# Performance work log

Measured on AMD Instinct MI355X. Metric: run time of the kernel, lower is better.

Reference implementation:

```python
import jax, jax.numpy as jnp
import numpy as np
import math

B, S, D_MODEL, NHEAD, DFF = 4, 1024, 1024, 16, 4096
D_K = D_MODEL // NHEAD
EPS = 1e-5
FACTOR = 5  # ProbAttention factor


def setup_inputs() -> dict:
    key = jax.random.key(0)
    ks = jax.random.split(key, 16)
    def w(k, shape):
        return 0.02 * jax.random.normal(k, shape, jnp.float32)
    inp = {
        "tgt": jax.random.normal(ks[0], (B, S, D_MODEL), jnp.float32),
        "memory": jax.random.normal(ks[1], (B, S, D_MODEL), jnp.float32),
    }
    i = 2
    for n in ["sa_wq", "sa_wk", "sa_wv", "sa_wo", "ca_wq", "ca_wk", "ca_wv", "ca_wo"]:
        inp[n] = w(ks[i], (D_MODEL, D_MODEL)); i += 1
        inp[n.replace("_w", "_b")] = jnp.zeros((D_MODEL,), jnp.float32)
    inp["w1"] = w(ks[i], (D_MODEL, DFF)); i += 1
    inp["b1"] = jnp.zeros((DFF,), jnp.float32)
    inp["w2"] = w(ks[i], (DFF, D_MODEL)); i += 1
    inp["b2"] = jnp.zeros((D_MODEL,), jnp.float32)
    for j in (1, 2, 3):
        inp[f"bn{j}_g"] = jnp.ones((D_MODEL,), jnp.float32)
        inp[f"bn{j}_b"] = jnp.zeros((D_MODEL,), jnp.float32)
    return inp


def prob_attention(q, k, v, rng):
    # Informer ProbSparse attention, mask_flag=False. q,k,v: [B,H,L,D]
    Bq, H, Lq, D = q.shape
    Lk = k.shape[2]
    sample_k = min(FACTOR * int(math.ceil(math.log(Lk))), Lk)
    n_top = min(FACTOR * int(math.ceil(math.log(Lq))), Lq)
    # sampled key indices per query position (shared across B,H, as in Informer)
    idx = jax.random.randint(rng, (Lq, sample_k), 0, Lk)
    k_samp = k[:, :, idx, :]                                 # [B,H,Lq,sample_k,D]
    qk_samp = jnp.einsum("bhld,bhlsd->bhls", q, k_samp)
    M = qk_samp.max(-1) - qk_samp.sum(-1) / Lk               # sparsity measure [B,H,Lq]
    top_idx = jax.lax.top_k(M, n_top)[1]                     # [B,H,n_top]
    q_red = jnp.take_along_axis(q, top_idx[..., None], axis=2)  # [B,H,n_top,D]
    scores = jnp.einsum("bhud,bhkd->bhuk", q_red, k) * (1.0 / math.sqrt(D))
    attn = jax.nn.softmax(scores, axis=-1)                   # [B,H,n_top,Lk]
    # initial context: mean of V for all queries, then overwrite the top queries
    ctx = jnp.broadcast_to(v.mean(axis=2, keepdims=True), (Bq, H, Lq, D))
    upd = jnp.einsum("bhuk,bhkd->bhud", attn, v)
    b_ix = jnp.arange(Bq)[:, None, None]
    h_ix = jnp.arange(H)[None, :, None]
    return ctx.at[b_ix, h_ix, top_idx].set(upd)


def mha(xq, xk, xv, wq, bq, wk, bk, wv, bv, wo, bo, rng):
    Bq, L, E = xq.shape
    def split(x, wt, bt):
        return (x @ wt + bt).reshape(Bq, L, NHEAD, D_K).transpose(0, 2, 1, 3)
    q, k, v = split(xq, wq, bq), split(xk, wk, bk), split(xv, wv, bv)
    o = prob_attention(q, k, v, rng)
    return o.transpose(0, 2, 1, 3).reshape(Bq, L, E) @ wo + bo


def bn(x, g, b):
    # BatchNorm1d over channel dim E, stats over (B, S) (training-mode, biased var)
    mu = x.mean(axis=(0, 1))
    var = x.var(axis=(0, 1))
    return (x - mu) * jax.lax.rsqrt(var + EPS) * g + b


def reference(tgt, memory, sa_wq, sa_bq, sa_wk, sa_bk, sa_wv, sa_bv, sa_wo, sa_bo,
              ca_wq, ca_bq, ca_wk, ca_bk, ca_wv, ca_bv, ca_wo, ca_bo,
              w1, b1, w2, b2, bn1_g, bn1_b, bn2_g, bn2_b, bn3_g, bn3_b):
    k1, k2 = jax.random.split(jax.random.key(42))
    t2 = mha(tgt, tgt, tgt, sa_wq, sa_bq, sa_wk, sa_bk, sa_wv, sa_bv, sa_wo, sa_bo, k1)
    x = bn(tgt + t2, bn1_g, bn1_b)
    t2 = mha(x, memory, memory, ca_wq, ca_bq, ca_wk, ca_bk, ca_wv, ca_bv, ca_wo, ca_bo, k2)
    x = bn(x + t2, bn2_g, bn2_b)
    t2 = jax.nn.gelu(x @ w1 + b1, approximate=False) @ w2 + b2
    return bn(x + t2, bn3_g, bn3_b)
```

## Files before the change

### kernel.cpp

```cpp
#include <hip/hip_runtime.h>
#include <cstdint>

#define BQ 4
#define SEQ 1024
#define EMB 1024
#define NH 16
#define DKH 64
#define DFF 4096
#define MROWS 4096
#define NSAMP 35
#define QKV_LD 3072

typedef int   i32x4 __attribute__((ext_vector_type(4)));
typedef float f32x4 __attribute__((ext_vector_type(4)));
typedef short s16x8 __attribute__((ext_vector_type(8)));
typedef __bf16 b16x8 __attribute__((ext_vector_type(8)));

__device__ __forceinline__ unsigned short bf16b(float f) {
  unsigned u = __builtin_bit_cast(unsigned, f);
  return (unsigned short)((u + 0x7FFFu + ((u >> 16) & 1u)) >> 16);
}

template <typename T> struct other_vec { using type = b16x8; };
template <> struct other_vec<b16x8>    { using type = s16x8; };

template <typename T>
__device__ __forceinline__ auto mfma_try(T a, T b, f32x4 c, int)
    -> decltype(__builtin_amdgcn_mfma_f32_16x16x32_bf16(a, b, c, 0, 0, 0)) {
  return __builtin_amdgcn_mfma_f32_16x16x32_bf16(a, b, c, 0, 0, 0);
}
template <typename T>
__device__ __forceinline__ f32x4 mfma_try(T a, T b, f32x4 c, long) {
  using U = typename other_vec<T>::type;
  U a2 = __builtin_bit_cast(U, a);
  U b2 = __builtin_bit_cast(U, b);
  return __builtin_amdgcn_mfma_f32_16x16x32_bf16(a2, b2, c, 0, 0, 0);
}
__device__ __forceinline__ f32x4 mfma_bf16(i32x4 a, i32x4 b, f32x4 c) {
  s16x8 as = __builtin_bit_cast(s16x8, a);
  s16x8 bs = __builtin_bit_cast(s16x8, b);
  return mfma_try(as, bs, c, 0);
}

typedef const __attribute__((address_space(1))) void GV;
typedef __attribute__((address_space(3))) void LV;
__device__ __forceinline__ void gload_lds16(const void* g, void* l) {
  __builtin_amdgcn_global_load_lds((GV*)(uintptr_t)g,
                                   (LV*)(unsigned)(uintptr_t)l, 16, 0, 0);
}

__device__ __forceinline__ void tf2x32(unsigned k0, unsigned k1, unsigned x0, unsigned x1,
                                       unsigned& o0, unsigned& o1) {
  unsigned ks2 = k0 ^ k1 ^ 0x1BD11BDAu;
  x0 += k0; x1 += k1;
#define TFR(r) { x0 += x1; x1 = (x1 << r) | (x1 >> (32 - r)); x1 ^= x0; }
  TFR(13) TFR(15) TFR(26) TFR(6)   x0 += k1;  x1 += ks2 + 1u;
  TFR(17) TFR(29) TFR(16) TFR(24)  x0 += ks2; x1 += k0 + 2u;
  TFR(13) TFR(15) TFR(26) TFR(6)   x0 += k0;  x1 += k1 + 3u;
  TFR(17) TFR(29) TFR(16) TFR(24)  x0 += k1;  x1 += ks2 + 4u;
  TFR(13) TFR(15) TFR(26) TFR(6)   x0 += ks2; x1 += k0 + 5u;
#undef TFR
  o0 = x0; o1 = x1;
}

__global__ void idx_kernel(int* __restrict__ out) {
  int t = blockIdx.x * 256 + threadIdx.x;
  if (t >= 2 * SEQ * NSAMP) return;
  int sel = t >= SEQ * NSAMP;
  int i = sel ? t - SEQ * NSAMP : t;
  unsigned s0, s1, d0, d1;
  tf2x32(0u, 42u, 0u, 0u, s0, s1);
  tf2x32(0u, 42u, 0u, 1u, d0, d1);
  unsigned key0 = sel ? d0 : s0, key1 = sel ? d1 : s1;
  unsigned o0, o1;
  tf2x32(key0, key1, 0u, (unsigned)i, o0, o1);
  out[t] = (int)((o0 ^ o1) & 1023u);
}

__global__ void f2b_kernel(const float* __restrict__ in, unsigned short* __restrict__ out, int n4) {
  int i = blockIdx.x * 256 + threadIdx.x;
  if (i >= n4) return;
  float4 v = ((const float4*)in)[i];
  uint2 p;
  p.x = (unsigned)bf16b(v.x) | ((unsigned)bf16b(v.y) << 16);
  p.y = (unsigned)bf16b(v.z) | ((unsigned)bf16b(v.w) << 16);
  ((uint2*)out)[i] = p;
}

__global__ void transpose_kernel(const float* __restrict__ W, unsigned short* __restrict__ WT,
                                 int K, int N) {
  __shared__ float tile[32][33];
  int n0 = blockIdx.x * 32, k0 = blockIdx.y * 32;
  int tx = threadIdx.x, ty = threadIdx.y;
#pragma unroll
  for (int r = 0; r < 4; ++r)
    tile[ty * 4 + r][tx] = W[(size_t)(k0 + ty * 4 + r) * N + n0 + tx];
  __syncthreads();
#pragma unroll
  for (int r = 0; r < 4; ++r) {
    int n = n0 + ty * 4 + r, k = k0 + tx;
    WT[(size_t)n * K + k] = bf16b(tile[tx][ty * 4 + r]);
  }
}

__global__ void biascat_kernel(const float* q, const float* k, const float* v,
                               const float* ck, const float* cv,
                               float* qkvB, float* kvB) {
  int t = blockIdx.x * 256 + threadIdx.x;
  if (t < 1024) {
    qkvB[t] = q[t]; qkvB[1024 + t] = k[t]; qkvB[2048 + t] = v[t];
    kvB[t] = ck[t]; kvB[1024 + t] = cv[t];
  }
}

template <int EPI>
__global__ __launch_bounds__(256) void gemm_kernel(
    const unsigned short* __restrict__ A, int lda,
    const unsigned short* __restrict__ BT, int ldb,
    float* __restrict__ C, int ldc,
    unsigned short* __restrict__ Cb, int ldcb,
    const float* __restrict__ bias, int K, int colofs) {
  __shared__ alignas(16) unsigned short As[128 * 32];
  __shared__ alignas(16) unsigned short Bs[128 * 32];
  const int tid = threadIdx.x;
  const int bm = blockIdx.y << 7, bn = blockIdx.x << 7;
  const int wave = tid >> 6, lane = tid & 63;
  const int wm = (wave & 1) << 6, wn = (wave >> 1) << 6;
  const int lr = lane & 15, lg = lane >> 4;

  f32x4 acc[4][4];
#pragma unroll
  for (int i = 0; i < 4; ++i)
#pragma unroll
    for (int j = 0; j < 4; ++j) acc[i][j] = f32x4{0.f, 0.f, 0.f, 0.f};

  const int trow = tid >> 2, tcol = (tid & 3) << 3;
  const unsigned short* Ag = A + (size_t)(bm + trow) * lda + tcol;
  const unsigned short* Bg = BT + (size_t)(bn + trow) * ldb + tcol;
  unsigned short* Al = &As[tid * 8];
  unsigned short* Bl = &Bs[tid * 8];

  for (int kt = 0; kt < K; kt += 32) {
    __syncthreads();
    gload_lds16(Ag + kt, Al);
    gload_lds16(Ag + (size_t)64 * lda + kt, Al + 2048);
    gload_lds16(Bg + kt, Bl);
    gload_lds16(Bg + (size_t)64 * ldb + kt, Bl + 2048);
    __syncthreads();
    i32x4 af[4], bf[4];
#pragma unroll
    for (int i = 0; i < 4; ++i)
      af[i] = *(const i32x4*)&As[(wm + i * 16 + lr) * 32 + lg * 8];
#pragma unroll
    for (int j = 0; j < 4; ++j)
      bf[j] = *(const i32x4*)&Bs[(wn + j * 16 + lr) * 32 + lg * 8];
#pragma unroll
    for (int i = 0; i < 4; ++i)
#pragma unroll
      for (int j = 0; j < 4; ++j)
        acc[i][j] = mfma_bf16(af[i], bf[j], acc[i][j]);
  }
#pragma unroll
  for (int i = 0; i < 4; ++i)
#pragma unroll
    for (int j = 0; j < 4; ++j)
#pragma unroll
      for (int r = 0; r < 4; ++r) {
        int row = bm + wm + i * 16 + lg * 4 + r;
        int col = bn + wn + j * 16 + lr;
        float v = acc[i][j][r] + bias[col];
        if constexpr (EPI == 0) {
          C[(size_t)row * ldc + col] = v;
        } else if constexpr (EPI == 1) {
          float gl = 0.5f * v * (1.f + erff(v * 0.70710678118654752f));
          Cb[(size_t)row * ldcb + col] = bf16b(gl);
        } else {
          int cc = col + colofs;
          int which = cc >> 10;
          int h = (cc >> 6) & 15;
          int d = col & 63;
          int b = row >> 10, l = row & 1023;
          C[((size_t)which << 22) + (((b << 4) + h) << 16) + (l << 6) + d] = v;
        }
      }
}

__global__ __launch_bounds__(256) void m3_kernel(
    const float* __restrict__ Qh, const float* __restrict__ Kh,
    const int* __restrict__ idx, float* __restrict__ Mout) {
  const int id = blockIdx.x;
  const int xcd = id & 7, slot = id >> 3;
  const int bh = xcd * 8 + (slot & 7), qc = slot >> 3;
  const int tid = threadIdx.x, wv = tid >> 6, lane = tid & 63;
  const float* Qb = Qh + ((size_t)bh << 16);
  const float* Kb = Kh + ((size_t)bh << 16);
  const bool act = lane < NSAMP;
  for (int j = 0; j < 32; ++j) {
    int l = qc * 128 + wv * 32 + j;
    float dot = 0.f;
    if (act) {
      int sidx = idx[l * NSAMP + lane];
      const float* Kr = Kb + ((size_t)sidx << 6);
      const float* Qr = Qb + ((size_t)l << 6);
#pragma unroll
      for (int d4 = 0; d4 < 16; ++d4) {
        float4 k4 = *(const float4*)(Kr + d4 * 4);
        float4 q4 = *(const float4*)(Qr + d4 * 4);
        dot = fmaf(k4.x, q4.x, dot);
        dot = fmaf(k4.y, q4.y, dot);
        dot = fmaf(k4.z, q4.z, dot);
        dot = fmaf(k4.w, q4.w, dot);
      }
    }
    float mval = act ? dot : -__builtin_inff();
    float sval = act ? dot : 0.f;
#pragma unroll
    for (int m = 1; m < 64; m <<= 1) {
      mval = fmaxf(mval, __shfl_xor(mval, m, 64));
      sval += __shfl_xor(sval, m, 64);
    }
    if (lane == 0) Mout[bh * 1024 + l] = mval - sval * (1.f / 1024.f);
  }
}

__device__ __forceinline__ void amax2(float& v, int& id, float v2, int id2) {
  if (v2 > v || (v2 == v && id2 < id)) { v = v2; id = id2; }
}
__global__ __launch_bounds__(64) void topk2_kernel(
    const float* __restrict__ Mbuf, int* __restrict__ topOut) {
  const int bh = blockIdx.x, t = threadIdx.x;
  float v[16]; int li[16];
#pragma unroll
  for (int r = 0; r < 16; ++r) { int l = t + (r << 6); v[r] = Mbuf[bh * 1024 + l]; li[r] = l; }
  for (int it = 0; it < NSAMP; ++it) {
    float bv = v[0]; int bi = li[0];
#pragma unroll
    for (int r = 1; r < 16; ++r) amax2(bv, bi, v[r], li[r]);
#pragma unroll
    for (int m = 1; m < 64; m <<= 1) {
      float ov = __shfl_xor(bv, m, 64); int oi = __shfl_xor(bi, m, 64);
      amax2(bv, bi, ov, oi);
    }
    if (t == 0) topOut[bh * NSAMP + it] = bi;
#pragma unroll
    for (int r = 0; r < 16; ++r) if (li[r] == bi) v[r] = -__builtin_inff();
  }
}

__global__ void vmean_kernel(const float* __restrict__ Vh, float* __restrict__ vmean) {
  const int g = blockIdx.x, bh = g >> 3, ch = g & 7;
  const int d = threadIdx.x;
  const float* Vb = Vh + ((size_t)bh << 16) + (ch * 128 << 6) + d;
  float s = 0.f;
  for (int l = 0; l < 128; ++l) s += Vb[l << 6];
  atomicAdd(&vmean[bh * 64 + d], s);
}

__global__ void fillO_kernel(const float* __restrict__ vmean, unsigned short* __restrict__ Ob) {
  int i = blockIdx.x * 256 + threadIdx.x;
  int e = i & 1023, b = i >> 20;
  int h = e >> 6, d = e & 63;
  Ob[i] = bf16b(vmean[((b << 4) + h) * 64 + d] * (1.f / 1024.f));
}

__global__ __launch_bounds__(256) void attn_part_kernel(
    const float* __restrict__ Qh, const float* __restrict__ Kh, const float* __restrict__ Vh,
    const int* __restrict__ topIdx, float* __restrict__ Opart) {
  __shared__ int til[NSAMP];
  __shared__ alignas(16) float qs[NSAMP * 64];
  __shared__ alignas(16) float ps[NSAMP * 260];
  const int id = blockIdx.x;
  const int xcd = id & 7, slot = id >> 3;
  const int bh = xcd * 8 + (slot & 7), c = slot >> 3;
  const int tid = threadIdx.x, wv = tid >> 6, lane = tid & 63;
  if (tid < NSAMP) til[tid] = topIdx[bh * NSAMP + tid];
  __syncthreads();
  for (int e = tid; e < NSAMP * 64; e += 256) {
    int i = e >> 6, d = e & 63;
    qs[e] = Qh[((size_t)bh << 16) + ((size_t)til[i] << 6) + d];
  }
  __syncthreads();
  {
    const float* Kr = Kh + ((size_t)bh << 16) + ((size_t)(c * 256 + tid) << 6);
    float acc[NSAMP];
#pragma unroll
    for (int i = 0; i < NSAMP; ++i) acc[i] = 0.f;
    for (int c16 = 0; c16 < 16; ++c16) {
      float4 k4 = *(const float4*)(Kr + c16 * 4);
#pragma unroll
      for (int i = 0; i < NSAMP; ++i) {
        float4 q4 = *(const float4*)&qs[i * 64 + c16 * 4];
        acc[i] = fmaf(k4.x, q4.x, acc[i]);
        acc[i] = fmaf(k4.y, q4.y, acc[i]);
        acc[i] = fmaf(k4.z, q4.z, acc[i]);
        acc[i] = fmaf(k4.w, q4.w, acc[i]);
      }
    }
#pragma unroll
    for (int i = 0; i < NSAMP; ++i) ps[i * 260 + tid] = expf(acc[i] * 0.125f);
  }
  __syncthreads();
  float o[NSAMP], sacc[NSAMP];
#pragma unroll
  for (int i = 0; i < NSAMP; ++i) { o[i] = 0.f; sacc[i] = 0.f; }
  {
    const float* Vb = Vh + ((size_t)bh << 16) + ((size_t)(c * 256) << 6) + lane;
    for (int j = 0; j < 64; ++j) {
      int kkl = wv * 64 + j;
      float vv = Vb[(size_t)kkl << 6];
#pragma unroll
      for (int i = 0; i < NSAMP; ++i) {
        float p = ps[i * 260 + kkl];
        o[i] = fmaf(p, vv, o[i]);
        sacc[i] += p;
      }
    }
  }
  __syncthreads();
  float* red = ps;
#pragma unroll
  for (int i = 0; i < NSAMP; ++i) {
    red[(wv * NSAMP + i) * 65 + lane] = o[i];
    if (lane == 0) red[(wv * NSAMP + i) * 65 + 64] = sacc[i];
  }
  __syncthreads();
  for (int e = tid; e < NSAMP * 65; e += 256) {
    int i = e / 65, d = e - i * 65;
    float s = red[(0 * NSAMP + i) * 65 + d] + red[(1 * NSAMP + i) * 65 + d] +
              red[(2 * NSAMP + i) * 65 + d] + red[(3 * NSAMP + i) * 65 + d];
    Opart[((size_t)(bh * NSAMP + i) * 4 + c) * 65 + d] = s;
  }
}

__global__ __launch_bounds__(256) void attn_final_kernel(
    const float* __restrict__ Opart, const int* __restrict__ topIdx,
    unsigned short* __restrict__ Ob) {
  int e = blockIdx.x * 256 + threadIdx.x;
  int d = e & 63, r = e >> 6;
  int bh = r / NSAMP, i = r - bh * NSAMP;
  const float* base = Opart + (size_t)r * 4 * 65;
  float s = base[d] + base[65 + d] + base[130 + d] + base[195 + d];
  float den = base[64] + base[129] + base[194] + base[259];
  int b = bh >> 4, h = bh & 15;
  int til = topIdx[r];
  Ob[((size_t)b * SEQ + til) * EMB + h * 64 + d] = bf16b(s / den);
}

__global__ __launch_bounds__(256) void bnstats_kernel(
    const float* __restrict__ a, const float* __restrict__ bb, float* __restrict__ sums) {
  const int t = threadIdx.x, r0 = blockIdx.x << 5;
  float s1[4] = {0, 0, 0, 0}, s2[4] = {0, 0, 0, 0};
  for (int r = r0; r < r0 + 32; ++r) {
    const float* ar = a + (size_t)r * EMB;
    const float* br = bb + (size_t)r * EMB;
#pragma unroll
    for (int q = 0; q < 4; ++q) {
      float x = ar[t + (q << 8)] + br[t + (q << 8)];
      s1[q] += x; s2[q] = fmaf(x, x, s2[q]);
    }
  }
#pragma unroll
  for (int q = 0; q < 4; ++q) {
    atomicAdd(&sums[t + (q << 8)], s1[q]);
    atomicAdd(&sums[EMB + t + (q << 8)], s2[q]);
  }
}
__global__ void bnapply_kernel(
    const float* __restrict__ a, const float* __restrict__ bres,
    const float* __restrict__ sums, const float* __restrict__ g,
    const float* __restrict__ bet, float* __restrict__ outF, unsigned short* __restrict__ outB) {
  int i = blockIdx.x * 256 + threadIdx.x;
  int c = i & (EMB - 1);
  float mu = sums[c] * (1.f / 4096.f);
  float var = sums[EMB + c] * (1.f / 4096.f) - mu * mu;
  float x = a[i] + bres[i];
  float y = (x - mu) * rsqrtf(var + 1e-5f) * g[c] + bet[c];
  outF[i] = y;
  if (outB) outB[i] = bf16b(y);
}

extern "C" void kernel_launch(void* const* d_in, const int* in_sizes, int n_in,
                              void* d_out, int out_size, void* d_ws, size_t ws_size,
                              hipStream_t stream) {
  const float* tgt  = (const float*)d_in[0];
  const float* memi = (const float*)d_in[1];
  const float* sa_wq = (const float*)d_in[2];  const float* sa_bq = (const float*)d_in[3];
  const float* sa_wk = (const float*)d_in[4];  const float* sa_bk = (const float*)d_in[5];
  const float* sa_wv = (const float*)d_in[6];  const float* sa_bv = (const float*)d_in[7];
  const float* sa_wo = (const float*)d_in[8];  const float* sa_bo = (const float*)d_in[9];
  const float* ca_wq = (const float*)d_in[10]; const float* ca_bq = (const float*)d_in[11];
  const float* ca_wk = (const float*)d_in[12]; const float* ca_bk = (const float*)d_in[13];
  const float* ca_wv = (const float*)d_in[14]; const float* ca_bv = (const float*)d_in[15];
  const float* ca_wo = (const float*)d_in[16]; const float* ca_bo = (const float*)d_in[17];
  const float* w1 = (const float*)d_in[18];    const float* b1 = (const float*)d_in[19];
  const float* w2 = (const float*)d_in[20];    const float* b2 = (const float*)d_in[21];
  const float* bn1g = (const float*)d_in[22];  const float* bn1b = (const float*)d_in[23];
  const float* bn2g = (const float*)d_in[24];  const float* bn2b = (const float*)d_in[25];
  const float* bn3g = (const float*)d_in[26];  const float* bn3b = (const float*)d_in[27];

  char* wsb = (char*)d_ws;
  size_t off = 0;
  auto alloc = [&](size_t bytes) -> char* {
    char* p = wsb + off;
    off = (off + bytes + 255) & ~(size_t)255;
    return p;
  };
  unsigned short* WTqkv = (unsigned short*)alloc((size_t)3072 * 1024 * 2);
  unsigned short* WTosa = (unsigned short*)alloc((size_t)1024 * 1024 * 2);
  unsigned short* WTqca = (unsigned short*)alloc((size_t)1024 * 1024 * 2);
  unsigned short* WTkv  = (unsigned short*)alloc((size_t)2048 * 1024 * 2);
  unsigned short* WToca = (unsigned short*)alloc((size_t)1024 * 1024 * 2);
  unsigned short* WT1   = (unsigned short*)alloc((size_t)4096 * 1024 * 2);
  unsigned short* WT2   = (unsigned short*)alloc((size_t)1024 * 4096 * 2);
  float* qkvB = (float*)alloc(3072 * 4);
  float* kvB  = (float*)alloc(2048 * 4);
  unsigned short* tgtB = (unsigned short*)alloc((size_t)MROWS * EMB * 2);
  unsigned short* memB = (unsigned short*)alloc((size_t)MROWS * EMB * 2);
  unsigned short* x1B  = (unsigned short*)alloc((size_t)MROWS * EMB * 2);
  unsigned short* x2B  = (unsigned short*)alloc((size_t)MROWS * EMB * 2);
  unsigned short* OB   = (unsigned short*)alloc((size_t)MROWS * EMB * 2);
  unsigned short* HB   = (unsigned short*)alloc((size_t)MROWS * DFF * 2);
  float* QKVh = (float*)alloc((size_t)3 * 64 * 65536 * 4);
  float* t2  = (float*)alloc((size_t)MROWS * EMB * 4);
  float* x1f = (float*)alloc((size_t)MROWS * EMB * 4);
  float* x2f = (float*)alloc((size_t)MROWS * EMB * 4);
  int* idxb  = (int*)alloc((size_t)2 * SEQ * NSAMP * 4);
  float* Mbuf = (float*)alloc((size_t)64 * 1024 * 4);
  int* topA = (int*)alloc(64 * NSAMP * 4);
  int* topB = (int*)alloc(64 * NSAMP * 4);
  float* vmean = (float*)alloc(64 * 64 * 4);
  float* sums = (float*)alloc(2 * EMB * 4);
  float* Opart = (float*)alloc((size_t)64 * NSAMP * 4 * 65 * 4);
  if (off > ws_size) return;

  float* Qh = QKVh;
  float* Kh = QKVh + ((size_t)1 << 22);
  float* Vh = QKVh + ((size_t)2 << 22);

  auto GEMM = [&](const unsigned short* A, int lda, const unsigned short* BT, int ldb,
                  float* C, int ldc, const float* bias, int M_, int N_, int K_) {
    dim3 g(N_ >> 7, M_ >> 7);
    gemm_kernel<0><<<g, 256, 0, stream>>>(A, lda, BT, ldb, C, ldc, nullptr, 0, bias, K_, 0);
  };
  auto GEMMG = [&](const unsigned short* A, int lda, const unsigned short* BT, int ldb,
                   unsigned short* Cb, int ldcb, const float* bias, int M_, int N_, int K_) {
    dim3 g(N_ >> 7, M_ >> 7);
    gemm_kernel<1><<<g, 256, 0, stream>>>(A, lda, BT, ldb, nullptr, 0, Cb, ldcb, bias, K_, 0);
  };
  auto GEMMH = [&](const unsigned short* A, const unsigned short* BT,
                   const float* bias, int N_, int K_, int colofs) {
    dim3 g(N_ >> 7, MROWS >> 7);
    gemm_kernel<2><<<g, 256, 0, stream>>>(A, K_, BT, K_, QKVh, 0, nullptr, 0, bias, K_, colofs);
  };
  auto TR = [&](const float* src, unsigned short* dst, int K_, int N_) {
    dim3 g(N_ / 32, K_ / 32), bl(32, 8);
    transpose_kernel<<<g, bl, 0, stream>>>(src, dst, K_, N_);
  };
  auto ATTN = [&](const int* top) {
    (void)hipMemsetAsync(vmean, 0, 64 * 64 * 4, stream);
    vmean_kernel<<<512, 64, 0, stream>>>(Vh, vmean);
    fillO_kernel<<<16384, 256, 0, stream>>>(vmean, OB);
    attn_part_kernel<<<256, 256, 0, stream>>>(Qh, Kh, Vh, top, Opart);
    attn_final_kernel<<<560, 256, 0, stream>>>(Opart, top, OB);
  };

  idx_kernel<<<280, 256, 0, stream>>>(idxb);
  f2b_kernel<<<4096, 256, 0, stream>>>(tgt, tgtB, MROWS * EMB / 4);
  f2b_kernel<<<4096, 256, 0, stream>>>(memi, memB, MROWS * EMB / 4);
  TR(sa_wq, WTqkv, 1024, 1024);
  TR(sa_wk, WTqkv + (size_t)1024 * 1024, 1024, 1024);
  TR(sa_wv, WTqkv + (size_t)2048 * 1024, 1024, 1024);
  TR(sa_wo, WTosa, 1024, 1024);
  TR(ca_wq, WTqca, 1024, 1024);
  TR(ca_wk, WTkv, 1024, 1024);
  TR(ca_wv, WTkv + (size_t)1024 * 1024, 1024, 1024);
  TR(ca_wo, WToca, 1024, 1024);
  TR(w1, WT1, 1024, 4096);
  TR(w2, WT2, 4096, 1024);
  biascat_kernel<<<4, 256, 0, stream>>>(sa_bq, sa_bk, sa_bv, ca_bk, ca_bv, qkvB, kvB);

  GEMMH(tgtB, WTqkv, qkvB, 3072, 1024, 0);
  m3_kernel<<<512, 256, 0, stream>>>(Qh, Kh, idxb, Mbuf);
  topk2_kernel<<<64, 64, 0, stream>>>(Mbuf, topA);
  ATTN(topA);
  GEMM(OB, 1024, WTosa, 1024, t2, 1024, sa_bo, MROWS, 1024, 1024);
  (void)hipMemsetAsync(sums, 0, 2 * EMB * 4, stream);
  bnstats_kernel<<<128, 256, 0, stream>>>(tgt, t2, sums);
  bnapply_kernel<<<16384, 256, 0, stream>>>(tgt, t2, sums, bn1g, bn1b, x1f, x1B);

  GEMMH(x1B, WTqca, ca_bq, 1024, 1024, 0);
  GEMMH(memB, WTkv, kvB, 2048, 1024, 1024);
  m3_kernel<<<512, 256, 0, stream>>>(Qh, Kh, idxb + SEQ * NSAMP, Mbuf);
  topk2_kernel<<<64, 64, 0, stream>>>(Mbuf, topB);
  ATTN(topB);
  GEMM(OB, 1024, WToca, 1024, t2, 1024, ca_bo, MROWS, 1024, 1024);
  (void)hipMemsetAsync(sums, 0, 2 * EMB * 4, stream);
  bnstats_kernel<<<128, 256, 0, stream>>>(x1f, t2, sums);
  bnapply_kernel<<<16384, 256, 0, stream>>>(x1f, t2, sums, bn2g, bn2b, x2f, x2B);

  GEMMG(x2B, 1024, WT1, 1024, HB, DFF, b1, MROWS, DFF, 1024);
  GEMM(HB, 4096, WT2, 4096, t2, 1024, b2, MROWS, 1024, 4096);
  (void)hipMemsetAsync(sums, 0, 2 * EMB * 4, stream);
  bnstats_kernel<<<128, 256, 0, stream>>>(x2f, t2, sums);
  bnapply_kernel<<<16384, 256, 0, stream>>>(x2f, t2, sums, bn3g, bn3b, (float*)d_out, nullptr);
}
```

Baseline: 984.0 us.

## Add 256x256-tile GEMM for QKV and FFN1, restructure sparsity-measure kernel

Adds a 512-thread GEMM with 256x256 output tiles and double-buffered LDS staging, used for the self-attention QKV projection and the first FFN GEMM to raise per-block data reuse. It also replaces the sparsity-measure kernel with one that assigns one query per wave across many more blocks, reducing partial dots through shared memory instead of full-wave shuffles. The larger tiles give few blocks for some shapes (48 and 256 blocks) and need many accumulator registers, which can hurt occupancy on a 256-CU device.

New measurement: 983.4 us. About the same (-0.1%).

```diff
diff --git a/kernel.cpp b/kernel.cpp
--- a/kernel.cpp
+++ b/kernel.cpp
@@ -185,41 +185,122 @@
       }
 }
 
-__global__ __launch_bounds__(256) void m3_kernel(
+template <int EPI>
+__global__ __launch_bounds__(512, 2) void gemm256_kernel(
+    const unsigned short* __restrict__ A, int lda,
+    const unsigned short* __restrict__ BT, int ldb,
+    float* __restrict__ C, int ldc,
+    unsigned short* __restrict__ Cb, int ldcb,
+    const float* __restrict__ bias, int K, int colofs) {
+  __shared__ alignas(16) unsigned short As2[2][256 * 32];
+  __shared__ alignas(16) unsigned short Bs2[2][256 * 32];
+  const int tid = threadIdx.x;
+  const int bm = blockIdx.y << 8, bn = blockIdx.x << 8;
+  const int wave = tid >> 6, lane = tid & 63;
+  const int wm2 = (wave >> 2) << 7;
+  const int wn4 = (wave & 3) << 6;
+  const int lr = lane & 15, lg = lane >> 4;
+
+  f32x4 acc[8][4];
+#pragma unroll
+  for (int i = 0; i < 8; ++i)
+#pragma unroll
+    for (int j = 0; j < 4; ++j) acc[i][j] = f32x4{0.f, 0.f, 0.f, 0.f};
+
+  const int srow = tid >> 2, scol = (tid & 3) << 3;
+  auto STAGE = [&](int sb, int kt) {
+#pragma unroll
+    for (int p = 0; p < 2; ++p) {
+      int rr = p * 128 + srow;
+      gload_lds16(A + (size_t)(bm + rr) * lda + kt + scol,
+                  &As2[sb][(size_t)(p * 512 + tid) * 8]);
+      gload_lds16(BT + (size_t)(bn + rr) * ldb + kt + scol,
+                  &Bs2[sb][(size_t)(p * 512 + tid) * 8]);
+    }
+  };
+
+  STAGE(0, 0);
+  __syncthreads();
+  int buf = 0;
+  for (int kt = 0; kt < K; kt += 32) {
+    if (kt + 32 < K) STAGE(buf ^ 1, kt + 32);
+    i32x4 af[8], bfr[4];
+#pragma unroll
+    for (int i = 0; i < 8; ++i)
+      af[i] = *(const i32x4*)&As2[buf][(wm2 + i * 16 + lr) * 32 + lg * 8];
+#pragma unroll
+    for (int j = 0; j < 4; ++j)
+      bfr[j] = *(const i32x4*)&Bs2[buf][(wn4 + j * 16 + lr) * 32 + lg * 8];
+#pragma unroll
+    for (int i = 0; i < 8; ++i)
+#pragma unroll
+      for (int j = 0; j < 4; ++j)
+        acc[i][j] = mfma_bf16(af[i], bfr[j], acc[i][j]);
+    __syncthreads();
+    buf ^= 1;
+  }
+#pragma unroll
+  for (int i = 0; i < 8; ++i)
+#pragma unroll
+    for (int j = 0; j < 4; ++j)
+#pragma unroll
+      for (int r = 0; r < 4; ++r) {
+        int row = bm + wm2 + i * 16 + lg * 4 + r;
+        int col = bn + wn4 + j * 16 + lr;
+        float v = acc[i][j][r] + bias[col];
+        if constexpr (EPI == 0) {
+          C[(size_t)row * ldc + col] = v;
+        } else if constexpr (EPI == 1) {
+          float gl = 0.5f * v * (1.f + erff(v * 0.70710678118654752f));
+          Cb[(size_t)row * ldcb + col] = bf16b(gl);
+        } else {
+          int cc = col + colofs;
+          int which = cc >> 10;
+          int h = (cc >> 6) & 15;
+          int d = col & 63;
+          int b = row >> 10, l = row & 1023;
+          C[((size_t)which << 22) + (((b << 4) + h) << 16) + (l << 6) + d] = v;
+        }
+      }
+}
+
+__global__ __launch_bounds__(256) void m5_kernel(
     const float* __restrict__ Qh, const float* __restrict__ Kh,
     const int* __restrict__ idx, float* __restrict__ Mout) {
-  const int id = blockIdx.x;
-  const int xcd = id & 7, slot = id >> 3;
-  const int bh = xcd * 8 + (slot & 7), qc = slot >> 3;
+  __shared__ float dots[4][36];
+  const int bh = blockIdx.x >> 8;
+  const int qbase = (blockIdx.x & 255) << 2;
   const int tid = threadIdx.x, wv = tid >> 6, lane = tid & 63;
-  const float* Qb = Qh + ((size_t)bh << 16);
-  const float* Kb = Kh + ((size_t)bh << 16);
-  const bool act = lane < NSAMP;
-  for (int j = 0; j < 32; ++j) {
-    int l = qc * 128 + wv * 32 + j;
-    float dot = 0.f;
-    if (act) {
-      int sidx = idx[l * NSAMP + lane];
-      const float* Kr = Kb + ((size_t)sidx << 6);
-      const float* Qr = Qb + ((size_t)l << 6);
-#pragma unroll
-      for (int d4 = 0; d4 < 16; ++d4) {
-        float4 k4 = *(const float4*)(Kr + d4 * 4);
-        float4 q4 = *(const float4*)(Qr + d4 * 4);
-        dot = fmaf(k4.x, q4.x, dot);
-        dot = fmaf(k4.y, q4.y, dot);
-        dot = fmaf(k4.z, q4.z, dot);
-        dot = fmaf(k4.w, q4.w, dot);
-      }
-    }
-    float mval = act ? dot : -__builtin_inff();
-    float sval = act ? dot : 0.f;
-#pragma unroll
-    for (int m = 1; m < 64; m <<= 1) {
-      mval = fmaxf(mval, __shfl_xor(mval, m, 64));
-      sval += __shfl_xor(sval, m, 64);
-    }
-    if (lane == 0) Mout[bh * 1024 + l] = mval - sval * (1.f / 1024.f);
+  const int l = qbase + wv;
+  const float* Qr = Qh + ((size_t)bh << 16) + ((size_t)l << 6);
+  if (lane < NSAMP) {
+    const int s = idx[l * NSAMP + lane];
+    const float* Kr = Kh + ((size_t)bh << 16) + ((size_t)s << 6);
+    float pa[4] = {0.f, 0.f, 0.f, 0.f};
+#pragma unroll
+    for (int d4 = 0; d4 < 16; ++d4) {
+      float4 k4 = *(const float4*)(Kr + d4 * 4);
+      float4 q4 = *(const float4*)(Qr + d4 * 4);
+      pa[d4 & 3] = fmaf(k4.x, q4.x, pa[d4 & 3]);
+      pa[d4 & 3] = fmaf(k4.y, q4.y, pa[d4 & 3]);
+      pa[d4 & 3] = fmaf(k4.z, q4.z, pa[d4 & 3]);
+      pa[d4 & 3] = fmaf(k4.w, q4.w, pa[d4 & 3]);
+    }
+    dots[wv][lane] = (pa[0] + pa[1]) + (pa[2] + pa[3]);
+  }
+  __syncthreads();
+  if (tid < 16) {
+    int q = tid >> 2, cp = tid & 3;
+    int sb = cp * 9, se = (cp == 3) ? NSAMP : (sb + 9);
+    float mx = -__builtin_inff(), sm = 0.f;
+    for (int s = sb; s < se; ++s) {
+      float v = dots[q][s];
+      mx = fmaxf(mx, v);
+      sm += v;
+    }
+    mx = fmaxf(mx, __shfl_xor(mx, 1, 64)); sm += __shfl_xor(sm, 1, 64);
+    mx = fmaxf(mx, __shfl_xor(mx, 2, 64)); sm += __shfl_xor(sm, 2, 64);
+    if (cp == 0) Mout[bh * 1024 + qbase + q] = mx - sm * (1.f / 1024.f);
   }
 }
 
@@ -442,16 +523,6 @@
     dim3 g(N_ >> 7, M_ >> 7);
     gemm_kernel<0><<<g, 256, 0, stream>>>(A, lda, BT, ldb, C, ldc, nullptr, 0, bias, K_, 0);
   };
-  auto GEMMG = [&](const unsigned short* A, int lda, const unsigned short* BT, int ldb,
-                   unsigned short* Cb, int ldcb, const float* bias, int M_, int N_, int K_) {
-    dim3 g(N_ >> 7, M_ >> 7);
-    gemm_kernel<1><<<g, 256, 0, stream>>>(A, lda, BT, ldb, nullptr, 0, Cb, ldcb, bias, K_, 0);
-  };
-  auto GEMMH = [&](const unsigned short* A, const unsigned short* BT,
-                   const float* bias, int N_, int K_, int colofs) {
-    dim3 g(N_ >> 7, MROWS >> 7);
-    gemm_kernel<2><<<g, 256, 0, stream>>>(A, K_, BT, K_, QKVh, 0, nullptr, 0, bias, K_, colofs);
-  };
   auto TR = [&](const float* src, unsigned short* dst, int K_, int N_) {
     dim3 g(N_ / 32, K_ / 32), bl(32, 8);
     transpose_kernel<<<g, bl, 0, stream>>>(src, dst, K_, N_);
@@ -479,8 +550,9 @@
   TR(w2, WT2, 4096, 1024);
   biascat_kernel<<<4, 256, 0, stream>>>(sa_bq, sa_bk, sa_bv, ca_bk, ca_bv, qkvB, kvB);
 
-  GEMMH(tgtB, WTqkv, qkvB, 3072, 1024, 0);
-  m3_kernel<<<512, 256, 0, stream>>>(Qh, Kh, idxb, Mbuf);
+  gemm256_kernel<2><<<dim3(3072 >> 8, MROWS >> 8), 512, 0, stream>>>(
+      tgtB, 1024, WTqkv, 1024, QKVh, 0, nullptr, 0, qkvB, 1024, 0);
+  m5_kernel<<<16384, 256, 0, stream>>>(Qh, Kh, idxb, Mbuf);
   topk2_kernel<<<64, 64, 0, stream>>>(Mbuf, topA);
   ATTN(topA);
   GEMM(OB, 1024, WTosa, 1024, t2, 1024, sa_bo, MROWS, 1024, 1024);
@@ -488,9 +560,11 @@
   bnstats_kernel<<<128, 256, 0, stream>>>(tgt, t2, sums);
   bnapply_kernel<<<16384, 256, 0, stream>>>(tgt, t2, sums, bn1g, bn1b, x1f, x1B);
 
-  GEMMH(x1B, WTqca, ca_bq, 1024, 1024, 0);
-  GEMMH(memB, WTkv, kvB, 2048, 1024, 1024);
-  m3_kernel<<<512, 256, 0, stream>>>(Qh, Kh, idxb + SEQ * NSAMP, Mbuf);
+  gemm_kernel<2><<<dim3(1024 >> 7, MROWS >> 7), 256, 0, stream>>>(
+      x1B, 1024, WTqca, 1024, QKVh, 0, nullptr, 0, ca_bq, 1024, 0);
+  gemm_kernel<2><<<dim3(2048 >> 7, MROWS >> 7), 256, 0, stream>>>(
+      memB, 1024, WTkv, 1024, QKVh, 0, nullptr, 0, kvB, 1024, 1024);
+  m5_kernel<<<16384, 256, 0, stream>>>(Qh, Kh, idxb + SEQ * NSAMP, Mbuf);
   topk2_kernel<<<64, 64, 0, stream>>>(Mbuf, topB);
   ATTN(topB);
   GEMM(OB, 1024, WToca, 1024, t2, 1024, ca_bo, MROWS, 1024, 1024);
@@ -498,7 +572,8 @@
   bnstats_kernel<<<128, 256, 0, stream>>>(x1f, t2, sums);
   bnapply_kernel<<<16384, 256, 0, stream>>>(x1f, t2, sums, bn2g, bn2b, x2f, x2B);
 
-  GEMMG(x2B, 1024, WT1, 1024, HB, DFF, b1, MROWS, DFF, 1024);
+  gemm256_kernel<1><<<dim3(DFF >> 8, MROWS >> 8), 512, 0, stream>>>(
+      x2B, 1024, WT1, 1024, nullptr, 0, HB, DFF, b1, 1024, 0);
   GEMM(HB, 4096, WT2, 4096, t2, 1024, b2, MROWS, 1024, 4096);
   (void)hipMemsetAsync(sums, 0, 2 * EMB * 4, stream);
   bnstats_kernel<<<128, 256, 0, stream>>>(x2f, t2, sums);
```

## Store head-split Q/K/V in bf16 and restructure sparsity-measure kernel

Applied to the files above, without the earlier changes.

The QKV projection epilogue now writes head-split Q, K and V as bf16 instead of fp32, and every consumer (sparsity measure, V mean, attention partials) unpacks bf16 on load. This halves the memory traffic for the intermediate QKV tensors. The M-measure kernel is rewritten so each block handles 4 queries with one wave per query, uses many more blocks, and reduces through shared memory. The bf16 rounding of Q/K can change which queries land in the top-k and slightly perturbs the attention outputs.

Result: faster. 870.4 us (-11.5%).

```diff
diff --git a/kernel.cpp b/kernel.cpp
--- a/kernel.cpp
+++ b/kernel.cpp
@@ -9,7 +9,6 @@
 #define DFF 4096
 #define MROWS 4096
 #define NSAMP 35
-#define QKV_LD 3072
 
 typedef int   i32x4 __attribute__((ext_vector_type(4)));
 typedef float f32x4 __attribute__((ext_vector_type(4)));
@@ -19,6 +18,15 @@
 __device__ __forceinline__ unsigned short bf16b(float f) {
   unsigned u = __builtin_bit_cast(unsigned, f);
   return (unsigned short)((u + 0x7FFFu + ((u >> 16) & 1u)) >> 16);
+}
+__device__ __forceinline__ float b2f(unsigned short v) {
+  return __builtin_bit_cast(float, (unsigned)v << 16);
+}
+__device__ __forceinline__ float blo(unsigned u) {
+  return __builtin_bit_cast(float, u << 16);
+}
+__device__ __forceinline__ float bhi(unsigned u) {
+  return __builtin_bit_cast(float, u & 0xFFFF0000u);
 }
 
 template <typename T> struct other_vec { using type = b16x8; };
@@ -180,46 +188,54 @@
           int h = (cc >> 6) & 15;
           int d = col & 63;
           int b = row >> 10, l = row & 1023;
-          C[((size_t)which << 22) + (((b << 4) + h) << 16) + (l << 6) + d] = v;
+          Cb[((size_t)which << 22) + (((b << 4) + h) << 16) + (l << 6) + d] = bf16b(v);
         }
       }
 }
 
-__global__ __launch_bounds__(256) void m3_kernel(
-    const float* __restrict__ Qh, const float* __restrict__ Kh,
+__global__ __launch_bounds__(256) void m6_kernel(
+    const unsigned short* __restrict__ Qh, const unsigned short* __restrict__ Kh,
     const int* __restrict__ idx, float* __restrict__ Mout) {
+  __shared__ float dots[4][36];
   const int id = blockIdx.x;
   const int xcd = id & 7, slot = id >> 3;
-  const int bh = xcd * 8 + (slot & 7), qc = slot >> 3;
+  const int bh = xcd * 8 + (slot & 7);
+  const int qbase = (slot >> 3) << 2;
   const int tid = threadIdx.x, wv = tid >> 6, lane = tid & 63;
-  const float* Qb = Qh + ((size_t)bh << 16);
-  const float* Kb = Kh + ((size_t)bh << 16);
-  const bool act = lane < NSAMP;
-  for (int j = 0; j < 32; ++j) {
-    int l = qc * 128 + wv * 32 + j;
-    float dot = 0.f;
-    if (act) {
-      int sidx = idx[l * NSAMP + lane];
-      const float* Kr = Kb + ((size_t)sidx << 6);
-      const float* Qr = Qb + ((size_t)l << 6);
-#pragma unroll
-      for (int d4 = 0; d4 < 16; ++d4) {
-        float4 k4 = *(const float4*)(Kr + d4 * 4);
-        float4 q4 = *(const float4*)(Qr + d4 * 4);
-        dot = fmaf(k4.x, q4.x, dot);
-        dot = fmaf(k4.y, q4.y, dot);
-        dot = fmaf(k4.z, q4.z, dot);
-        dot = fmaf(k4.w, q4.w, dot);
-      }
+  const int l = qbase + wv;
+  const unsigned short* Qr = Qh + ((size_t)bh << 16) + ((size_t)l << 6);
+  if (lane < NSAMP) {
+    const int s = idx[l * NSAMP + lane];
+    const unsigned short* Kr = Kh + ((size_t)bh << 16) + ((size_t)s << 6);
+    float pa0 = 0.f, pa1 = 0.f, pa2 = 0.f, pa3 = 0.f;
+#pragma unroll
+    for (int c8 = 0; c8 < 8; ++c8) {
+      uint4 kk = *(const uint4*)(Kr + c8 * 8);
+      uint4 qq = *(const uint4*)(Qr + c8 * 8);
+      pa0 = fmaf(blo(kk.x), blo(qq.x), pa0);
+      pa1 = fmaf(bhi(kk.x), bhi(qq.x), pa1);
+      pa2 = fmaf(blo(kk.y), blo(qq.y), pa2);
+      pa3 = fmaf(bhi(kk.y), bhi(qq.y), pa3);
+      pa0 = fmaf(blo(kk.z), blo(qq.z), pa0);
+      pa1 = fmaf(bhi(kk.z), bhi(qq.z), pa1);
+      pa2 = fmaf(blo(kk.w), blo(qq.w), pa2);
+      pa3 = fmaf(bhi(kk.w), bhi(qq.w), pa3);
     }
-    float mval = act ? dot : -__builtin_inff();
-    float sval = act ? dot : 0.f;
-#pragma unroll
-    for (int m = 1; m < 64; m <<= 1) {
-      mval = fmaxf(mval, __shfl_xor(mval, m, 64));
-      sval += __shfl_xor(sval, m, 64);
+    dots[wv][lane] = (pa0 + pa1) + (pa2 + pa3);
+  }
+  __syncthreads();
+  if (tid < 16) {
+    int q = tid >> 2, cp = tid & 3;
+    int sb = cp * 9, se = (cp == 3) ? NSAMP : (sb + 9);
+    float mx = -__builtin_inff(), sm = 0.f;
+    for (int s = sb; s < se; ++s) {
+      float v = dots[q][s];
+      mx = fmaxf(mx, v);
+      sm += v;
     }
-    if (lane == 0) Mout[bh * 1024 + l] = mval - sval * (1.f / 1024.f);
+    mx = fmaxf(mx, __shfl_xor(mx, 1, 64)); sm += __shfl_xor(sm, 1, 64);
+    mx = fmaxf(mx, __shfl_xor(mx, 2, 64)); sm += __shfl_xor(sm, 2, 64);
+    if (cp == 0) Mout[bh * 1024 + qbase + q] = mx - sm * (1.f / 1024.f);
   }
 }
 
@@ -247,12 +263,12 @@
   }
 }
 
-__global__ void vmean_kernel(const float* __restrict__ Vh, float* __restrict__ vmean) {
+__global__ void vmean_kernel(const unsigned short* __restrict__ Vh, float* __restrict__ vmean) {
   const int g = blockIdx.x, bh = g >> 3, ch = g & 7;
   const int d = threadIdx.x;
-  const float* Vb = Vh + ((size_t)bh << 16) + (ch * 128 << 6) + d;
+  const unsigned short* Vb = Vh + ((size_t)bh << 16) + (ch * 128 << 6) + d;
   float s = 0.f;
-  for (int l = 0; l < 128; ++l) s += Vb[l << 6];
+  for (int l = 0; l < 128; ++l) s += b2f(Vb[l << 6]);
   atomicAdd(&vmean[bh * 64 + d], s);
 }
 
@@ -264,7 +280,8 @@
 }
 
 __global__ __launch_bounds__(256) void attn_part_kernel(
-    const float* __restrict__ Qh, const float* __restrict__ Kh, const float* __restrict__ Vh,
+    const unsigned short* __restrict__ Qh, const unsigned short* __restrict__ Kh,
+    const unsigned short* __restrict__ Vh,
     const int* __restrict__ topIdx, float* __restrict__ Opart) {
   __shared__ int til[NSAMP];
   __shared__ alignas(16) float qs[NSAMP * 64];
@@ -277,23 +294,30 @@
   __syncthreads();
   for (int e = tid; e < NSAMP * 64; e += 256) {
     int i = e >> 6, d = e & 63;
-    qs[e] = Qh[((size_t)bh << 16) + ((size_t)til[i] << 6) + d];
+    qs[e] = b2f(Qh[((size_t)bh << 16) + ((size_t)til[i] << 6) + d]);
   }
   __syncthreads();
   {
-    const float* Kr = Kh + ((size_t)bh << 16) + ((size_t)(c * 256 + tid) << 6);
+    const unsigned short* Kr = Kh + ((size_t)bh << 16) + ((size_t)(c * 256 + tid) << 6);
     float acc[NSAMP];
 #pragma unroll
     for (int i = 0; i < NSAMP; ++i) acc[i] = 0.f;
-    for (int c16 = 0; c16 < 16; ++c16) {
-      float4 k4 = *(const float4*)(Kr + c16 * 4);
+    for (int c8 = 0; c8 < 8; ++c8) {
+      uint4 kk = *(const uint4*)(Kr + c8 * 8);
+      float k0 = blo(kk.x), k1 = bhi(kk.x), k2 = blo(kk.y), k3 = bhi(kk.y);
+      float k4 = blo(kk.z), k5 = bhi(kk.z), k6 = blo(kk.w), k7 = bhi(kk.w);
 #pragma unroll
       for (int i = 0; i < NSAMP; ++i) {
-        float4 q4 = *(const float4*)&qs[i * 64 + c16 * 4];
-        acc[i] = fmaf(k4.x, q4.x, acc[i]);
-        acc[i] = fmaf(k4.y, q4.y, acc[i]);
-        acc[i] = fmaf(k4.z, q4.z, acc[i]);
-        acc[i] = fmaf(k4.w, q4.w, acc[i]);
+        float4 qa = *(const float4*)&qs[i * 64 + c8 * 8];
+        float4 qb = *(const float4*)&qs[i * 64 + c8 * 8 + 4];
+        acc[i] = fmaf(k0, qa.x, acc[i]);
+        acc[i] = fmaf(k1, qa.y, acc[i]);
+        acc[i] = fmaf(k2, qa.z, acc[i]);
+        acc[i] = fmaf(k3, qa.w, acc[i]);
+        acc[i] = fmaf(k4, qb.x, acc[i]);
+        acc[i] = fmaf(k5, qb.y, acc[i]);
+        acc[i] = fmaf(k6, qb.z, acc[i]);
+        acc[i] = fmaf(k7, qb.w, acc[i]);
       }
     }
 #pragma unroll
@@ -304,10 +328,10 @@
 #pragma unroll
   for (int i = 0; i < NSAMP; ++i) { o[i] = 0.f; sacc[i] = 0.f; }
   {
-    const float* Vb = Vh + ((size_t)bh << 16) + ((size_t)(c * 256) << 6) + lane;
+    const unsigned short* Vb = Vh + ((size_t)bh << 16) + ((size_t)(c * 256) << 6) + lane;
     for (int j = 0; j < 64; ++j) {
       int kkl = wv * 64 + j;
-      float vv = Vb[(size_t)kkl << 6];
+      float vv = b2f(Vb[(size_t)kkl << 6]);
 #pragma unroll
       for (int i = 0; i < NSAMP; ++i) {
         float p = ps[i * 260 + kkl];
@@ -420,7 +444,7 @@
   unsigned short* x2B  = (unsigned short*)alloc((size_t)MROWS * EMB * 2);
   unsigned short* OB   = (unsigned short*)alloc((size_t)MROWS * EMB * 2);
   unsigned short* HB   = (unsigned short*)alloc((size_t)MROWS * DFF * 2);
-  float* QKVh = (float*)alloc((size_t)3 * 64 * 65536 * 4);
+  unsigned short* QKVhB = (unsigned short*)alloc((size_t)3 * 64 * 65536 * 2);
   float* t2  = (float*)alloc((size_t)MROWS * EMB * 4);
   float* x1f = (float*)alloc((size_t)MROWS * EMB * 4);
   float* x2f = (float*)alloc((size_t)MROWS * EMB * 4);
@@ -433,24 +457,19 @@
   float* Opart = (float*)alloc((size_t)64 * NSAMP * 4 * 65 * 4);
   if (off > ws_size) return;
 
-  float* Qh = QKVh;
-  float* Kh = QKVh + ((size_t)1 << 22);
-  float* Vh = QKVh + ((size_t)2 << 22);
+  unsigned short* Qh = QKVhB;
+  unsigned short* Kh = QKVhB + ((size_t)1 << 22);
+  unsigned short* Vh = QKVhB + ((size_t)2 << 22);
 
   auto GEMM = [&](const unsigned short* A, int lda, const unsigned short* BT, int ldb,
                   float* C, int ldc, const float* bias, int M_, int N_, int K_) {
     dim3 g(N_ >> 7, M_ >> 7);
     gemm_kernel<0><<<g, 256, 0, stream>>>(A, lda, BT, ldb, C, ldc, nullptr, 0, bias, K_, 0);
   };
-  auto GEMMG = [&](const unsigned short* A, int lda, const unsigned short* BT, int ldb,
-                   unsigned short* Cb, int ldcb, const float* bias, int M_, int N_, int K_) {
-    dim3 g(N_ >> 7, M_ >> 7);
-    gemm_kernel<1><<<g, 256, 0, stream>>>(A, lda, BT, ldb, nullptr, 0, Cb, ldcb, bias, K_, 0);
-  };
   auto GEMMH = [&](const unsigned short* A, const unsigned short* BT,
                    const float* bias, int N_, int K_, int colofs) {
     dim3 g(N_ >> 7, MROWS >> 7);
-    gemm_kernel<2><<<g, 256, 0, stream>>>(A, K_, BT, K_, QKVh, 0, nullptr, 0, bias, K_, colofs);
+    gemm_kernel<2><<<g, 256, 0, stream>>>(A, K_, BT, K_, nullptr, 0, QKVhB, 0, bias, K_, colofs);
   };
   auto TR = [&](const float* src, unsigned short* dst, int K_, int N_) {
     dim3 g(N_ / 32, K_ / 32), bl(32, 8);
@@ -480,7 +499,7 @@
   biascat_kernel<<<4, 256, 0, stream>>>(sa_bq, sa_bk, sa_bv, ca_bk, ca_bv, qkvB, kvB);
 
   GEMMH(tgtB, WTqkv, qkvB, 3072, 1024, 0);
-  m3_kernel<<<512, 256, 0, stream>>>(Qh, Kh, idxb, Mbuf);
+  m6_kernel<<<16384, 256, 0, stream>>>(Qh, Kh, idxb, Mbuf);
   topk2_kernel<<<64, 64, 0, stream>>>(Mbuf, topA);
   ATTN(topA);
   GEMM(OB, 1024, WTosa, 1024, t2, 1024, sa_bo, MROWS, 1024, 1024);
@@ -490,7 +509,7 @@
 
   GEMMH(x1B, WTqca, ca_bq, 1024, 1024, 0);
   GEMMH(memB, WTkv, kvB, 2048, 1024, 1024);
-  m3_kernel<<<512, 256, 0, stream>>>(Qh, Kh, idxb + SEQ * NSAMP, Mbuf);
+  m6_kernel<<<16384, 256, 0, stream>>>(Qh, Kh, idxb + SEQ * NSAMP, Mbuf);
   topk2_kernel<<<64, 64, 0, stream>>>(Mbuf, topB);
   ATTN(topB);
   GEMM(OB, 1024, WToca, 1024, t2, 1024, ca_bo, MROWS, 1024, 1024);
@@ -498,7 +517,8 @@
   bnstats_kernel<<<128, 256, 0, stream>>>(x1f, t2, sums);
   bnapply_kernel<<<16384, 256, 0, stream>>>(x1f, t2, sums, bn2g, bn2b, x2f, x2B);
 
-  GEMMG(x2B, 1024, WT1, 1024, HB, DFF, b1, MROWS, DFF, 1024);
+  gemm_kernel<1><<<dim3(DFF >> 7, MROWS >> 7), 256, 0, stream>>>(
+      x2B, 1024, WT1, 1024, nullptr, 0, HB, DFF, b1, 1024, 0);
   GEMM(HB, 4096, WT2, 4096, t2, 1024, b2, MROWS, 1024, 4096);
   (void)hipMemsetAsync(sums, 0, 2 * EMB * 4, stream);
   bnstats_kernel<<<128, 256, 0, stream>>>(x2f, t2, sums);
```
